# Kernel optimization log

Hardware: AMD Instinct MI355X
Metric: run time of the kernel (lower is better)

## Reference

```python
import jax, jax.numpy as jnp
import numpy as np

N_E = 1024
E_DIM = 256
BETA = 0.25
EPS = 1e-10


def setup_inputs() -> dict:
    key = jax.random.key(0)
    k1, k2 = jax.random.split(key)
    z = jax.random.normal(k1, (32, E_DIM, 32, 32), dtype=jnp.float32)
    emb = jax.random.normal(k2, (N_E, E_DIM), dtype=jnp.float32)
    return {"z": z, "emb": emb}


def reference(z, emb):
    sg = jax.lax.stop_gradient
    # (B, C, H, W) -> (B, H, W, C)
    zp = jnp.transpose(z, (0, 2, 3, 1))
    zf = zp.reshape(-1, E_DIM)  # (N, C), N = B*H*W
    # squared euclidean distances: ||z||^2 + ||e||^2 - 2 z e^T  -> (N, n_e)
    d = (jnp.sum(zf * zf, axis=1, keepdims=True)
         + jnp.sum(emb * emb, axis=1)
         - 2.0 * jnp.matmul(zf, emb.T))
    idx = jnp.argmin(d, axis=1)  # (N,)
    # one-hot @ codebook == gather (same math, no dense one-hot matmul)
    z_q1 = emb[idx].reshape(zp.shape)  # (B, H, W, C)
    # loss: note original does NOT detach z_q1 anywhere
    loss = jnp.mean((z_q1 - zp) ** 2) + BETA * jnp.mean((z_q1 - sg(zp)) ** 2)
    # straight-through (original detaches z, not z_q1)
    z_q = zp + (z_q1 - sg(zp))
    # perplexity from mean one-hot encodings = normalized histogram of indices
    counts = jnp.bincount(idx, length=N_E)
    e_mean = counts.astype(zf.dtype) / idx.shape[0]
    perplexity = jnp.exp(-jnp.sum(e_mean * jnp.log(e_mean + EPS)))
    z_q = jnp.transpose(z_q, (0, 3, 1, 2))
    z_q1_out = jnp.transpose(z_q1, (0, 3, 1, 2))
    return loss, z_q, perplexity, idx, z_q1_out
```

## Files before the change

### kernel.cpp

```cpp
#include <hip/hip_runtime.h>
#include <hip/hip_bf16.h>
#include <math.h>

#define CDIM 256
#define HW   1024
#define NVEC 32768
#define NE   1024
#define ZSIZE 8388608
#define NSPLIT 2
#define MARGIN 0.075f

#define OUT_LOSS 0
#define OUT_ZQ   1
#define OUT_PERP 8388609
#define OUT_IDX  8388610
#define OUT_ZQ1  8421378

#define WS_LOSS   0
#define WS_RCNT   64
#define WS_HIST   128
#define WS_ENORM  4224
#define WS_IDX    8448
#define WS_RLIST  139520
#define WS_S1     270592
#define WS_S2     532736
#define WS_J1     794880
#define WS_EBH    1057024
#define WS_EBL    1581312
#define WS_ZBH    2105600
#define WS_ZBL    18882816
#define WS_SCORE  WS_EBL

typedef __attribute__((ext_vector_type(8))) short short8;
typedef __attribute__((ext_vector_type(4))) float f32x4;
typedef __attribute__((ext_vector_type(8))) unsigned short ushort8v;
typedef __attribute__((ext_vector_type(8))) _Float16 half8;

__device__ __forceinline__ unsigned short f16_rne(float x) {
    _Float16 h = (_Float16)x;
    return __builtin_bit_cast(unsigned short, h);
}
__device__ __forceinline__ float f16_to_f(unsigned short u) {
    return (float)__builtin_bit_cast(_Float16, u);
}
__device__ __forceinline__ void lds_barrier() {
    asm volatile("s_waitcnt lgkmcnt(0)\n\ts_barrier" ::: "memory");
}

__global__ __launch_bounds__(256) void vq_prep(
    const float* __restrict__ z, const float* __restrict__ emb,
    unsigned short* __restrict__ zbh, unsigned short* __restrict__ zbl,
    unsigned short* __restrict__ ebh, float* __restrict__ enorm)
{
    const int tid = threadIdx.x, w = tid >> 6, L = tid & 63;
    if (blockIdx.x < 512) {
        __shared__ unsigned short th[64 * 264];
        __shared__ unsigned short tl[64 * 264];
        const int b = blockIdx.x >> 4, hw0 = (blockIdx.x & 15) << 6;
        const float* zp = z + (size_t)b * (CDIM * HW) + hw0;
        for (int i = 0; i < 16; ++i) {
            int k = (i * 4 + w) * 4;
            float f0 = zp[(size_t)(k + 0) * HW + L];
            float f1 = zp[(size_t)(k + 1) * HW + L];
            float f2 = zp[(size_t)(k + 2) * HW + L];
            float f3 = zp[(size_t)(k + 3) * HW + L];
            ushort4 hi = { f16_rne(f0), f16_rne(f1), f16_rne(f2), f16_rne(f3) };
            ushort4 lo = { f16_rne(f0 - f16_to_f(hi.x)), f16_rne(f1 - f16_to_f(hi.y)),
                           f16_rne(f2 - f16_to_f(hi.z)), f16_rne(f3 - f16_to_f(hi.w)) };
            *(ushort4*)&th[L * 264 + k] = hi;
            *(ushort4*)&tl[L * 264 + k] = lo;
        }
        __syncthreads();
#pragma unroll
        for (int it = 0; it < 8; ++it) {
            int row = it * 8 + (tid >> 5);
            int kc = (tid & 31) * 8;
            size_t o = (size_t)(b * 1024 + hw0 + row) * CDIM + kc;
            *(ushort8v*)(zbh + o) = *(ushort8v*)&th[row * 264 + kc];
            *(ushort8v*)(zbl + o) = *(ushort8v*)&tl[row * 264 + kc];
        }
    } else {
        const int cb = (int)(blockIdx.x - 512) * 64;
        for (int p = 0; p < 16; ++p) {
            int code = cb + p * 4 + w;
            float4 v = *(const float4*)(emb + (size_t)code * CDIM + L * 4);
            float s = v.x * v.x + v.y * v.y + v.z * v.z + v.w * v.w;
            for (int off = 32; off; off >>= 1) s += __shfl_down(s, off, 64);
            if (L == 0) enorm[code] = s;
            ushort4 hi = { f16_rne(v.x), f16_rne(v.y), f16_rne(v.z), f16_rne(v.w) };
            *(ushort4*)(ebh + (size_t)code * CDIM + L * 4) = hi;
        }
    }
}

__global__ __launch_bounds__(256, 2) void vq_mfma3(
    const unsigned short* __restrict__ zbh, const unsigned short* __restrict__ zbl,
    const unsigned short* __restrict__ ebh,
    const float* __restrict__ enorm,
    float* __restrict__ s1_ws, float* __restrict__ s2_ws, int* __restrict__ j1_ws)
{
    __shared__ short albuf[32768];
    __shared__ short bbuf[2][4096];

    const int tid = threadIdx.x, w = tid >> 6, L = tid & 63;
    const int l15 = L & 15, q = L >> 4;
    const int r16 = tid & 15, ch = (tid >> 4) & 3;
    const int mtile = blockIdx.x & 255, js = blockIdx.x >> 8;
    const int n0 = mtile << 7;
    const int jsbase = js << 9;

#pragma unroll
    for (int ro = 0; ro < 16; ++ro) {
        const int seg = ro * 4 + w;
        const int sw2 = seg >> 4, smf = (seg >> 3) & 1, skk = seg & 7;
        short8 v = *(const short8*)(zbl + (size_t)(n0 + sw2 * 32 + smf * 16 + r16) * CDIM + skk * 32 + ch * 8);
        *(short8*)(albuf + seg * 512 + L * 8) = v;
    }
    half8 AH[2][8];
#pragma unroll
    for (int mf = 0; mf < 2; ++mf)
#pragma unroll
        for (int kk = 0; kk < 8; ++kk)
            AH[mf][kk] = *(const half8*)(zbh + (size_t)(n0 + w * 32 + mf * 16 + l15) * CDIM + kk * 32 + q * 8);
    __syncthreads();

    float s1[2][4], s2[2][4]; int j1[2][4];
#pragma unroll
    for (int mf = 0; mf < 2; ++mf)
#pragma unroll
        for (int r = 0; r < 4; ++r) { s1[mf][r] = -3.4e38f; s2[mf][r] = -3.4e38f; j1[mf][r] = 0; }

    short8 st[2];
#pragma unroll
    for (int ro = 0; ro < 2; ++ro)
        st[ro] = *(const short8*)(ebh + (size_t)(jsbase + (ro * 4 + w) * 16 + r16) * CDIM + ch * 8);
#pragma unroll
    for (int ro = 0; ro < 2; ++ro)
        *(short8*)(bbuf[0] + (ro * 4 + w) * 512 + L * 8) = st[ro];
#pragma unroll
    for (int ro = 0; ro < 2; ++ro)
        st[ro] = *(const short8*)(ebh + (size_t)(jsbase + (ro * 4 + w) * 16 + r16) * CDIM + 32 + ch * 8);
    lds_barrier();

    f32x4 acc[2][8];
#pragma unroll 8
    for (int t = 0; t < 32; ++t) {
        const int kk = t & 7;
        if (kk == 0) {
#pragma unroll
            for (int mf = 0; mf < 2; ++mf)
#pragma unroll
                for (int jf = 0; jf < 8; ++jf)
                    acc[mf][jf] = (f32x4){0.f, 0.f, 0.f, 0.f};
        }
        half8 AL0 = *(const half8*)(albuf + (w * 16 + kk) * 512 + L * 8);
        half8 AL1 = *(const half8*)(albuf + (w * 16 + 8 + kk) * 512 + L * 8);
        const short* bb = bbuf[t & 1];
#pragma unroll
        for (int jf = 0; jf < 8; ++jf) {
            half8 Bh = *(const half8*)(bb + jf * 512 + L * 8);
            acc[0][jf] = __builtin_amdgcn_mfma_f32_16x16x32_f16(AH[0][kk], Bh, acc[0][jf], 0, 0, 0);
            acc[1][jf] = __builtin_amdgcn_mfma_f32_16x16x32_f16(AH[1][kk], Bh, acc[1][jf], 0, 0, 0);
            acc[0][jf] = __builtin_amdgcn_mfma_f32_16x16x32_f16(AL0, Bh, acc[0][jf], 0, 0, 0);
            acc[1][jf] = __builtin_amdgcn_mfma_f32_16x16x32_f16(AL1, Bh, acc[1][jf], 0, 0, 0);
        }
        if (t < 31) {
#pragma unroll
            for (int ro = 0; ro < 2; ++ro)
                *(short8*)(bbuf[(t + 1) & 1] + (ro * 4 + w) * 512 + L * 8) = st[ro];
            if (t < 30) {
                const int t2 = t + 2;
                const int j0n = jsbase + (t2 >> 3) * 128;
                const int k0n = (t2 & 7) * 32;
#pragma unroll
                for (int ro = 0; ro < 2; ++ro)
                    st[ro] = *(const short8*)(ebh + (size_t)(j0n + (ro * 4 + w) * 16 + r16) * CDIM + k0n + ch * 8);
            }
            lds_barrier();
        }
        if (kk == 7) {
            const int j0 = jsbase + (t >> 3) * 128;
#pragma unroll
            for (int jf = 0; jf < 8; ++jf) {
                const int j = j0 + jf * 16 + l15;
                const float hn = 0.5f * enorm[j];
#pragma unroll
                for (int mf = 0; mf < 2; ++mf)
#pragma unroll
                    for (int r = 0; r < 4; ++r) {
                        float s = acc[mf][jf][r] - hn;
                        if (s > s1[mf][r]) { s2[mf][r] = s1[mf][r]; s1[mf][r] = s; j1[mf][r] = j; }
                        else if (s > s2[mf][r]) s2[mf][r] = s;
                    }
            }
        }
    }

#pragma unroll
    for (int mf = 0; mf < 2; ++mf)
#pragma unroll
        for (int r = 0; r < 4; ++r) {
            float a1 = s1[mf][r], a2 = s2[mf][r]; int aj = j1[mf][r];
            for (int m = 1; m < 16; m <<= 1) {
                float o1 = __shfl_xor(a1, m, 64);
                float o2 = __shfl_xor(a2, m, 64);
                int   oj = __shfl_xor(aj, m, 64);
                if (o1 > a1 || (o1 == a1 && oj < aj)) { a2 = fmaxf(a1, o2); a1 = o1; aj = oj; }
                else a2 = fmaxf(a2, o1);
            }
            if (l15 == 0) {
                int o = js * NVEC + n0 + w * 32 + mf * 16 + q * 4 + r;
                s1_ws[o] = a1; s2_ws[o] = a2; j1_ws[o] = aj;
            }
        }
}

__global__ __launch_bounds__(256) void vq_merge(
    const float* __restrict__ s1_ws, const float* __restrict__ s2_ws,
    const int* __restrict__ j1_ws, int* __restrict__ idx_ws,
    float* __restrict__ idx_out, int* __restrict__ hist,
    int* __restrict__ rcnt, int* __restrict__ rlist,
    unsigned long long* __restrict__ score)
{
    int n = blockIdx.x * 256 + threadIdx.x;
    score[n] = 0ull;
    float b1 = -3.4e38f, b2 = -3.4e38f; int bj = 0;
#pragma unroll
    for (int s = 0; s < NSPLIT; ++s) {
        float a1 = s1_ws[s * NVEC + n], a2 = s2_ws[s * NVEC + n];
        int aj = j1_ws[s * NVEC + n];
        if (a1 > b1 || (a1 == b1 && aj < bj)) { b2 = fmaxf(b1, a2); b1 = a1; bj = aj; }
        else b2 = fmaxf(b2, a1);
    }
    idx_ws[n] = bj;
    if (b1 - b2 < MARGIN) {
        int p = atomicAdd(rcnt, 1); rlist[p] = n;
    } else {
        idx_out[n] = (float)bj;
        atomicAdd(&hist[bj], 1);
    }
}

__global__ __launch_bounds__(256) void vq_rescue(
    const float* __restrict__ z, const float* __restrict__ emb,
    const float* __restrict__ enorm, const int* __restrict__ rcnt,
    const int* __restrict__ rlist, unsigned long long* __restrict__ score)
{
    __shared__ __align__(16) float zrow[256];
    __shared__ float en_s[64];
    __shared__ float rs[4];
    __shared__ int   rj[4];
    const int tid = threadIdx.x;
    const int wv = tid >> 6, L = tid & 63;
    const int chunk = blockIdx.x & 15;
    const int jwave = chunk * 64 + wv * 16;
    const int jodd = L >> 5;
    const int rstride = gridDim.x >> 4;
    const int count = *rcnt;

    for (int it = blockIdx.x >> 4; it < count; it += rstride) {
        __syncthreads();
        const int n = rlist[it];
        zrow[tid] = z[(size_t)(n >> 10) * (CDIM * HW) + (size_t)tid * HW + (n & 1023)];
        if (tid < 64) en_s[tid] = enorm[chunk * 64 + tid];
        __syncthreads();
        const float4 zv = *(const float4*)&zrow[L * 4];

        float b1 = -3.4e38f; int bj = 0x7fffffff;
#pragma unroll
        for (int jo = 0; jo < 16; jo += 2) {
            const int jA = jwave + jo;
            const float4 eA = *(const float4*)(emb + (size_t)jA * CDIM + L * 4);
            const float4 eB = *(const float4*)(emb + (size_t)(jA + 1) * CDIM + L * 4);
            float pA = fmaf(zv.x, eA.x, fmaf(zv.y, eA.y, fmaf(zv.z, eA.z, zv.w * eA.w)));
            float pB = fmaf(zv.x, eB.x, fmaf(zv.y, eB.y, fmaf(zv.z, eB.z, zv.w * eB.w)));
            float tA = pA + __shfl_xor(pA, 32, 64);
            float tB = pB + __shfl_xor(pB, 32, 64);
            float u = (L < 32) ? tA : tB;
            u += __shfl_xor(u, 16, 64);
            u += __shfl_xor(u, 8, 64);
            u += __shfl_xor(u, 4, 64);
            u += __shfl_xor(u, 2, 64);
            u += __shfl_xor(u, 1, 64);
            const int j = jA + jodd;
            const float s = u - 0.5f * en_s[wv * 16 + jo + jodd];
            if (s > b1) { b1 = s; bj = j; }
        }
        {
            const float o1 = __shfl_xor(b1, 32, 64);
            const int   oj = __shfl_xor(bj, 32, 64);
            if (o1 > b1 || (o1 == b1 && oj < bj)) { b1 = o1; bj = oj; }
        }
        if (L == 0) { rs[wv] = b1; rj[wv] = bj; }
        __syncthreads();
        if (tid == 0) {
            float f1 = rs[0]; int fj = rj[0];
#pragma unroll
            for (int v = 1; v < 4; ++v)
                if (rs[v] > f1 || (rs[v] == f1 && rj[v] < fj)) { f1 = rs[v]; fj = rj[v]; }
            unsigned key = __float_as_uint(f1);
            key = (key & 0x80000000u) ? ~key : (key | 0x80000000u);
            unsigned long long packed = ((unsigned long long)key << 32) | (unsigned)(~fj);
            atomicMax(&score[it], packed);
        }
    }
}

__global__ __launch_bounds__(256) void vq_rfin(
    const int* __restrict__ rcnt, const int* __restrict__ rlist,
    const unsigned long long* __restrict__ score, int* __restrict__ idx_ws,
    float* __restrict__ idx_out, int* __restrict__ hist)
{
    const int count = *rcnt;
    for (int it = blockIdx.x * 256 + threadIdx.x; it < count; it += gridDim.x * 256) {
        const unsigned long long p = score[it];
        const int fj = (int)(~(unsigned)p) & (NE - 1);
        const int n = rlist[it];
        idx_ws[n] = fj;
        idx_out[n] = (float)fj;
        atomicAdd(&hist[fj], 1);
    }
}

__global__ __launch_bounds__(256) void vq_gather(
    const float* __restrict__ z, const float* __restrict__ emb,
    const int* __restrict__ idx_ws, float* __restrict__ zq,
    float* __restrict__ zq1, double* __restrict__ loss_sum)
{
    __shared__ float es[32 * 129];
    __shared__ int ids[32];
    __shared__ float wred[4];

    const int tid = threadIdx.x, w = tid >> 6, L = tid & 63;
    const int b   = blockIdx.x >> 6;
    const int half = (blockIdx.x >> 5) & 1;
    const int hw0 = (blockIdx.x & 31) << 5;
    const int n0  = (b << 10) + hw0;
    const int c0  = half << 7;

    if (tid < 32) ids[tid] = idx_ws[n0 + tid];
    __syncthreads();

#pragma unroll
    for (int p = 0; p < 4; ++p) {
        int u = p * 256 + tid;
        int r = u >> 5, cq = (u & 31) * 4;
        float4 v = *(const float4*)(emb + (size_t)ids[r] * CDIM + c0 + cq);
        es[r * 129 + cq + 0] = v.x;
        es[r * 129 + cq + 1] = v.y;
        es[r * 129 + cq + 2] = v.z;
        es[r * 129 + cq + 3] = v.w;
    }
    __syncthreads();

    const int row = L & 31, cp = L >> 5;
    const size_t zbase = (size_t)b * (CDIM * HW) + hw0 + row;
    float ls = 0.f;
    for (int rd = 0; rd < 16; ++rd) {
        int cl = rd * 8 + w * 2 + cp;
        size_t off = zbase + (size_t)(c0 + cl) * HW;
        float zv = z[off];
        float e  = es[row * 129 + cl];
        float d  = e - zv;
        zq[off]  = zv + d;
        zq1[off] = e;
        ls += d * d;
    }

    for (int off = 32; off; off >>= 1) ls += __shfl_down(ls, off, 64);
    if (L == 0) wred[w] = ls;
    __syncthreads();
    if (tid == 0)
        atomicAdd(loss_sum, (double)(wred[0] + wred[1] + wred[2] + wred[3]));
}

__global__ __launch_bounds__(1024) void vq_final(
    const int* __restrict__ hist, const double* __restrict__ loss_sum,
    float* __restrict__ out_loss, float* __restrict__ out_perp)
{
    int tid = threadIdx.x;
    float em = (float)hist[tid] * (1.0f / 32768.0f);
    float term = em * logf(em + 1e-10f);
    for (int off = 32; off; off >>= 1) term += __shfl_down(term, off, 64);
    __shared__ float red[16];
    int lane = tid & 63, wv = tid >> 6;
    if (lane == 0) red[wv] = term;
    __syncthreads();
    if (tid == 0) {
        float s = 0.f;
        for (int i = 0; i < 16; ++i) s += red[i];
        *out_perp = expf(-s);
        *out_loss = (float)(*loss_sum * 1.25 / 8388608.0);
    }
}

extern "C" void kernel_launch(void* const* d_in, const int* in_sizes, int n_in,
                              void* d_out, int out_size, void* d_ws, size_t ws_size,
                              hipStream_t stream) {
    const float* z   = (const float*)d_in[0];
    const float* emb = (const float*)d_in[1];
    float* out = (float*)d_out;
    char*  ws  = (char*)d_ws;

    double* loss_sum    = (double*)(ws + WS_LOSS);
    int*    rcnt        = (int*)(ws + WS_RCNT);
    int*    hist        = (int*)(ws + WS_HIST);
    float*  enorm       = (float*)(ws + WS_ENORM);
    int*    idx_ws      = (int*)(ws + WS_IDX);
    int*    rlist       = (int*)(ws + WS_RLIST);
    float*  s1_ws       = (float*)(ws + WS_S1);
    float*  s2_ws       = (float*)(ws + WS_S2);
    int*    j1_ws       = (int*)(ws + WS_J1);
    unsigned short* ebh = (unsigned short*)(ws + WS_EBH);
    unsigned short* zbh = (unsigned short*)(ws + WS_ZBH);
    unsigned short* zbl = (unsigned short*)(ws + WS_ZBL);
    unsigned long long* score = (unsigned long long*)(ws + WS_SCORE);

    hipMemsetAsync(d_ws, 0, 4224, stream);

    vq_prep  <<<528, 256, 0, stream>>>(z, emb, zbh, zbl, ebh, enorm);
    vq_mfma3 <<<512, 256, 0, stream>>>(zbh, zbl, ebh, enorm, s1_ws, s2_ws, j1_ws);
    vq_merge <<<128, 256, 0, stream>>>(s1_ws, s2_ws, j1_ws, idx_ws, out + OUT_IDX, hist, rcnt, rlist, score);
    vq_rescue<<<2048, 256, 0, stream>>>(z, emb, enorm, rcnt, rlist, score);
    vq_rfin  <<<8, 256, 0, stream>>>(rcnt, rlist, score, idx_ws, out + OUT_IDX, hist);
    vq_gather<<<2048, 256, 0, stream>>>(z, emb, idx_ws, out + OUT_ZQ, out + OUT_ZQ1, loss_sum);
    vq_final <<<1, 1024, 0, stream>>>(hist, loss_sum, out + OUT_LOSS, out + OUT_PERP);
}
```

Before: 230.5 us.

## Drop fp16 low-part split, widen rescue margin, split codebook four ways

Removes the hi/lo fp16 split of z, so the distance GEMM runs with a single fp16 MFMA pass instead of two, and the low-part buffer is no longer written or read. To make up for the lost precision, the rescue margin is widened from 0.075 to 0.18, so more near-tie vectors get recomputed exactly in fp32. The codebook is split 4 ways (1024 blocks, launch bounds 3) with a smaller B tile and code norms staged in LDS. The memset and the vq_rfin kernel are folded into vq_prep and vq_gather, and rescue results are now keyed by vector index. The risk is that a larger rescue set adds fp32 work, and that correctness depends on the wider margin covering the fp16 error.

```diff
diff --git a/kernel.cpp b/kernel.cpp
--- a/kernel.cpp
+++ b/kernel.cpp
@@ -7,8 +7,8 @@
 #define NVEC 32768
 #define NE   1024
 #define ZSIZE 8388608
-#define NSPLIT 2
-#define MARGIN 0.075f
+#define NSPLIT 4
+#define MARGIN 0.18f
 
 #define OUT_LOSS 0
 #define OUT_ZQ   1
@@ -23,13 +23,11 @@
 #define WS_IDX    8448
 #define WS_RLIST  139520
 #define WS_S1     270592
-#define WS_S2     532736
-#define WS_J1     794880
-#define WS_EBH    1057024
-#define WS_EBL    1581312
-#define WS_ZBH    2105600
-#define WS_ZBL    18882816
-#define WS_SCORE  WS_EBL
+#define WS_S2     794880
+#define WS_J1     1319168
+#define WS_SCORE  1843456
+#define WS_EBH    2105600
+#define WS_ZBH    2629888
 
 typedef __attribute__((ext_vector_type(8))) short short8;
 typedef __attribute__((ext_vector_type(4))) float f32x4;
@@ -40,22 +38,18 @@
     _Float16 h = (_Float16)x;
     return __builtin_bit_cast(unsigned short, h);
 }
-__device__ __forceinline__ float f16_to_f(unsigned short u) {
-    return (float)__builtin_bit_cast(_Float16, u);
-}
 __device__ __forceinline__ void lds_barrier() {
     asm volatile("s_waitcnt lgkmcnt(0)\n\ts_barrier" ::: "memory");
 }
 
 __global__ __launch_bounds__(256) void vq_prep(
     const float* __restrict__ z, const float* __restrict__ emb,
-    unsigned short* __restrict__ zbh, unsigned short* __restrict__ zbl,
-    unsigned short* __restrict__ ebh, float* __restrict__ enorm)
+    unsigned short* __restrict__ zbh, unsigned short* __restrict__ ebh,
+    float* __restrict__ enorm, int* __restrict__ wsz)
 {
     const int tid = threadIdx.x, w = tid >> 6, L = tid & 63;
     if (blockIdx.x < 512) {
         __shared__ unsigned short th[64 * 264];
-        __shared__ unsigned short tl[64 * 264];
         const int b = blockIdx.x >> 4, hw0 = (blockIdx.x & 15) << 6;
         const float* zp = z + (size_t)b * (CDIM * HW) + hw0;
         for (int i = 0; i < 16; ++i) {
@@ -65,10 +59,7 @@
             float f2 = zp[(size_t)(k + 2) * HW + L];
             float f3 = zp[(size_t)(k + 3) * HW + L];
             ushort4 hi = { f16_rne(f0), f16_rne(f1), f16_rne(f2), f16_rne(f3) };
-            ushort4 lo = { f16_rne(f0 - f16_to_f(hi.x)), f16_rne(f1 - f16_to_f(hi.y)),
-                           f16_rne(f2 - f16_to_f(hi.z)), f16_rne(f3 - f16_to_f(hi.w)) };
             *(ushort4*)&th[L * 264 + k] = hi;
-            *(ushort4*)&tl[L * 264 + k] = lo;
         }
         __syncthreads();
 #pragma unroll
@@ -77,9 +68,11 @@
             int kc = (tid & 31) * 8;
             size_t o = (size_t)(b * 1024 + hw0 + row) * CDIM + kc;
             *(ushort8v*)(zbh + o) = *(ushort8v*)&th[row * 264 + kc];
-            *(ushort8v*)(zbl + o) = *(ushort8v*)&tl[row * 264 + kc];
         }
     } else {
+        if (blockIdx.x == 512) {
+            for (int i = tid; i < 1056; i += 256) wsz[i] = 0;
+        }
         const int cb = (int)(blockIdx.x - 512) * 64;
         for (int p = 0; p < 16; ++p) {
             int code = cb + p * 4 + w;
@@ -93,36 +86,29 @@
     }
 }
 
-__global__ __launch_bounds__(256, 2) void vq_mfma3(
-    const unsigned short* __restrict__ zbh, const unsigned short* __restrict__ zbl,
-    const unsigned short* __restrict__ ebh,
+__global__ __launch_bounds__(256, 3) void vq_mfma3(
+    const unsigned short* __restrict__ zbh, const unsigned short* __restrict__ ebh,
     const float* __restrict__ enorm,
     float* __restrict__ s1_ws, float* __restrict__ s2_ws, int* __restrict__ j1_ws)
 {
-    __shared__ short albuf[32768];
-    __shared__ short bbuf[2][4096];
+    __shared__ short bbuf[2][2048];
+    __shared__ float en_s[256];
 
     const int tid = threadIdx.x, w = tid >> 6, L = tid & 63;
     const int l15 = L & 15, q = L >> 4;
     const int r16 = tid & 15, ch = (tid >> 4) & 3;
     const int mtile = blockIdx.x & 255, js = blockIdx.x >> 8;
     const int n0 = mtile << 7;
-    const int jsbase = js << 9;
-
-#pragma unroll
-    for (int ro = 0; ro < 16; ++ro) {
-        const int seg = ro * 4 + w;
-        const int sw2 = seg >> 4, smf = (seg >> 3) & 1, skk = seg & 7;
-        short8 v = *(const short8*)(zbl + (size_t)(n0 + sw2 * 32 + smf * 16 + r16) * CDIM + skk * 32 + ch * 8);
-        *(short8*)(albuf + seg * 512 + L * 8) = v;
-    }
+    const int jsbase = js << 8;
+
     half8 AH[2][8];
 #pragma unroll
     for (int mf = 0; mf < 2; ++mf)
 #pragma unroll
         for (int kk = 0; kk < 8; ++kk)
             AH[mf][kk] = *(const half8*)(zbh + (size_t)(n0 + w * 32 + mf * 16 + l15) * CDIM + kk * 32 + q * 8);
-    __syncthreads();
+
+    en_s[tid] = enorm[jsbase + tid];
 
     float s1[2][4], s2[2][4]; int j1[2][4];
 #pragma unroll
@@ -130,19 +116,16 @@
 #pragma unroll
         for (int r = 0; r < 4; ++r) { s1[mf][r] = -3.4e38f; s2[mf][r] = -3.4e38f; j1[mf][r] = 0; }
 
+    const unsigned short* ebase = ebh + (size_t)(jsbase + w * 16 + r16) * CDIM + ch * 8;
+
     short8 st[2];
-#pragma unroll
-    for (int ro = 0; ro < 2; ++ro)
-        st[ro] = *(const short8*)(ebh + (size_t)(jsbase + (ro * 4 + w) * 16 + r16) * CDIM + ch * 8);
-#pragma unroll
-    for (int ro = 0; ro < 2; ++ro)
-        *(short8*)(bbuf[0] + (ro * 4 + w) * 512 + L * 8) = st[ro];
-#pragma unroll
-    for (int ro = 0; ro < 2; ++ro)
-        st[ro] = *(const short8*)(ebh + (size_t)(jsbase + (ro * 4 + w) * 16 + r16) * CDIM + 32 + ch * 8);
+    st[0] = *(const short8*)(ebase);
+    *(short8*)(bbuf[0] + w * 512 + L * 8) = st[0];
+    st[1] = *(const short8*)(ebase + 32);
+    st[0] = *(const short8*)(ebase + 64);
     lds_barrier();
 
-    f32x4 acc[2][8];
+    f32x4 acc[2][4];
 #pragma unroll 8
     for (int t = 0; t < 32; ++t) {
         const int kk = t & 7;
@@ -150,40 +133,31 @@
 #pragma unroll
             for (int mf = 0; mf < 2; ++mf)
 #pragma unroll
-                for (int jf = 0; jf < 8; ++jf)
+                for (int jf = 0; jf < 4; ++jf)
                     acc[mf][jf] = (f32x4){0.f, 0.f, 0.f, 0.f};
         }
-        half8 AL0 = *(const half8*)(albuf + (w * 16 + kk) * 512 + L * 8);
-        half8 AL1 = *(const half8*)(albuf + (w * 16 + 8 + kk) * 512 + L * 8);
         const short* bb = bbuf[t & 1];
 #pragma unroll
-        for (int jf = 0; jf < 8; ++jf) {
-            half8 Bh = *(const half8*)(bb + jf * 512 + L * 8);
-            acc[0][jf] = __builtin_amdgcn_mfma_f32_16x16x32_f16(AH[0][kk], Bh, acc[0][jf], 0, 0, 0);
-            acc[1][jf] = __builtin_amdgcn_mfma_f32_16x16x32_f16(AH[1][kk], Bh, acc[1][jf], 0, 0, 0);
-            acc[0][jf] = __builtin_amdgcn_mfma_f32_16x16x32_f16(AL0, Bh, acc[0][jf], 0, 0, 0);
-            acc[1][jf] = __builtin_amdgcn_mfma_f32_16x16x32_f16(AL1, Bh, acc[1][jf], 0, 0, 0);
+        for (int jf = 0; jf < 4; ++jf) {
+            half8 B = *(const half8*)(bb + jf * 512 + L * 8);
+            acc[0][jf] = __builtin_amdgcn_mfma_f32_16x16x32_f16(AH[0][kk], B, acc[0][jf], 0, 0, 0);
+            acc[1][jf] = __builtin_amdgcn_mfma_f32_16x16x32_f16(AH[1][kk], B, acc[1][jf], 0, 0, 0);
         }
         if (t < 31) {
-#pragma unroll
-            for (int ro = 0; ro < 2; ++ro)
-                *(short8*)(bbuf[(t + 1) & 1] + (ro * 4 + w) * 512 + L * 8) = st[ro];
-            if (t < 30) {
-                const int t2 = t + 2;
-                const int j0n = jsbase + (t2 >> 3) * 128;
-                const int k0n = (t2 & 7) * 32;
-#pragma unroll
-                for (int ro = 0; ro < 2; ++ro)
-                    st[ro] = *(const short8*)(ebh + (size_t)(j0n + (ro * 4 + w) * 16 + r16) * CDIM + k0n + ch * 8);
+            *(short8*)(bbuf[(t + 1) & 1] + w * 512 + L * 8) = st[(t + 1) & 1];
+            if (t < 29) {
+                const int t3 = t + 3;
+                st[(t + 1) & 1] = *(const short8*)(ebase + (size_t)(t3 >> 3) * (64 * CDIM) + (t3 & 7) * 32);
             }
             lds_barrier();
         }
         if (kk == 7) {
-            const int j0 = jsbase + (t >> 3) * 128;
-#pragma unroll
-            for (int jf = 0; jf < 8; ++jf) {
-                const int j = j0 + jf * 16 + l15;
-                const float hn = 0.5f * enorm[j];
+            const int jg = t >> 3;
+#pragma unroll
+            for (int jf = 0; jf < 4; ++jf) {
+                const int jl = jg * 64 + jf * 16 + l15;
+                const int j = jsbase + jl;
+                const float hn = 0.5f * en_s[jl];
 #pragma unroll
                 for (int mf = 0; mf < 2; ++mf)
 #pragma unroll
@@ -232,10 +206,11 @@
         if (a1 > b1 || (a1 == b1 && aj < bj)) { b2 = fmaxf(b1, a2); b1 = a1; bj = aj; }
         else b2 = fmaxf(b2, a1);
     }
-    idx_ws[n] = bj;
     if (b1 - b2 < MARGIN) {
+        idx_ws[n] = -1;
         int p = atomicAdd(rcnt, 1); rlist[p] = n;
     } else {
+        idx_ws[n] = bj;
         idx_out[n] = (float)bj;
         atomicAdd(&hist[bj], 1);
     }
@@ -301,31 +276,17 @@
             unsigned key = __float_as_uint(f1);
             key = (key & 0x80000000u) ? ~key : (key | 0x80000000u);
             unsigned long long packed = ((unsigned long long)key << 32) | (unsigned)(~fj);
-            atomicMax(&score[it], packed);
-        }
-    }
-}
-
-__global__ __launch_bounds__(256) void vq_rfin(
-    const int* __restrict__ rcnt, const int* __restrict__ rlist,
-    const unsigned long long* __restrict__ score, int* __restrict__ idx_ws,
-    float* __restrict__ idx_out, int* __restrict__ hist)
-{
-    const int count = *rcnt;
-    for (int it = blockIdx.x * 256 + threadIdx.x; it < count; it += gridDim.x * 256) {
-        const unsigned long long p = score[it];
-        const int fj = (int)(~(unsigned)p) & (NE - 1);
-        const int n = rlist[it];
-        idx_ws[n] = fj;
-        idx_out[n] = (float)fj;
-        atomicAdd(&hist[fj], 1);
+            atomicMax(&score[n], packed);
+        }
     }
 }
 
 __global__ __launch_bounds__(256) void vq_gather(
     const float* __restrict__ z, const float* __restrict__ emb,
-    const int* __restrict__ idx_ws, float* __restrict__ zq,
-    float* __restrict__ zq1, double* __restrict__ loss_sum)
+    const int* __restrict__ idx_ws, const unsigned long long* __restrict__ score,
+    float* __restrict__ zq, float* __restrict__ zq1,
+    float* __restrict__ idx_out, int* __restrict__ hist,
+    double* __restrict__ loss_sum)
 {
     __shared__ float es[32 * 129];
     __shared__ int ids[32];
@@ -338,7 +299,18 @@
     const int n0  = (b << 10) + hw0;
     const int c0  = half << 7;
 
-    if (tid < 32) ids[tid] = idx_ws[n0 + tid];
+    if (tid < 32) {
+        const int n = n0 + tid;
+        int id = idx_ws[n];
+        if (id < 0) {
+            id = (int)(~(unsigned)score[n]) & (NE - 1);
+            if (half == 0) {
+                idx_out[n] = (float)id;
+                atomicAdd(&hist[id], 1);
+            }
+        }
+        ids[tid] = id;
+    }
     __syncthreads();
 
 #pragma unroll
@@ -413,16 +385,12 @@
     int*    j1_ws       = (int*)(ws + WS_J1);
     unsigned short* ebh = (unsigned short*)(ws + WS_EBH);
     unsigned short* zbh = (unsigned short*)(ws + WS_ZBH);
-    unsigned short* zbl = (unsigned short*)(ws + WS_ZBL);
     unsigned long long* score = (unsigned long long*)(ws + WS_SCORE);
 
-    hipMemsetAsync(d_ws, 0, 4224, stream);
-
-    vq_prep  <<<528, 256, 0, stream>>>(z, emb, zbh, zbl, ebh, enorm);
-    vq_mfma3 <<<512, 256, 0, stream>>>(zbh, zbl, ebh, enorm, s1_ws, s2_ws, j1_ws);
+    vq_prep  <<<528, 256, 0, stream>>>(z, emb, zbh, ebh, enorm, (int*)ws);
+    vq_mfma3 <<<1024, 256, 0, stream>>>(zbh, ebh, enorm, s1_ws, s2_ws, j1_ws);
     vq_merge <<<128, 256, 0, stream>>>(s1_ws, s2_ws, j1_ws, idx_ws, out + OUT_IDX, hist, rcnt, rlist, score);
     vq_rescue<<<2048, 256, 0, stream>>>(z, emb, enorm, rcnt, rlist, score);
-    vq_rfin  <<<8, 256, 0, stream>>>(rcnt, rlist, score, idx_ws, out + OUT_IDX, hist);
-    vq_gather<<<2048, 256, 0, stream>>>(z, emb, idx_ws, out + OUT_ZQ, out + OUT_ZQ1, loss_sum);
+    vq_gather<<<2048, 256, 0, stream>>>(z, emb, idx_ws, score, out + OUT_ZQ, out + OUT_ZQ1, out + OUT_IDX, hist, loss_sum);
     vq_final <<<1, 1024, 0, stream>>>(hist, loss_sum, out + OUT_LOSS, out + OUT_PERP);
 }
```

Measured after the change: 249.6 us. 1.08x slower.
